# Kernel optimization log

Hardware: AMD Instinct MI355X
Metric: run time of the kernel (lower is better)

## Reference

```python
import jax, jax.numpy as jnp
import numpy as np

N_NODES = 100000


def gcn_conv(x, W, b, src, dst, n_nodes):
    # Linear transform first (PyG GCNConv applies weight before propagation)
    h = x @ W  # [N, out]
    # gcn_norm with self-loops: deg[i] = 1 + #incoming edges at i
    ones = jnp.ones(src.shape[0], dtype=h.dtype)
    deg = jax.ops.segment_sum(ones, dst, num_segments=n_nodes) + 1.0
    dinv = jax.lax.rsqrt(deg)  # deg^{-1/2}, deg >= 1 so safe
    norm = dinv[src] * dinv[dst]  # [E]
    # aggregate normalized messages at destination nodes
    agg = jax.ops.segment_sum(h[src] * norm[:, None], dst, num_segments=n_nodes)
    # self-loop contribution: norm_ii = dinv[i]^2
    agg = agg + h * (dinv * dinv)[:, None]
    return agg + b


def setup_inputs() -> dict:
    key = jax.random.key(0)
    k1, k2, k3, k4, k5, k6 = jax.random.split(key, 6)
    num_features, hidden, num_classes = 512, 128, 64
    x = jax.random.normal(k1, (N_NODES, num_features), dtype=jnp.float32)
    edge_index = jax.random.randint(k2, (2, 1600000), 0, N_NODES, dtype=jnp.int64)
    # Glorot-style params (scaled normals)
    W1 = jax.random.normal(k3, (num_features, hidden), dtype=jnp.float32) / np.sqrt(num_features)
    b1 = jnp.zeros((hidden,), dtype=jnp.float32)
    W2 = jax.random.normal(k4, (hidden, num_classes), dtype=jnp.float32) / np.sqrt(hidden)
    b2 = jnp.zeros((num_classes,), dtype=jnp.float32)
    return {"x": x, "edge_index": edge_index, "W1": W1, "b1": b1, "W2": W2, "b2": b2}


def reference(x, edge_index, W1, b1, W2, b2):
    src, dst = edge_index[0], edge_index[1]
    h = jax.nn.relu(gcn_conv(x, W1, b1, src, dst, N_NODES))
    out = gcn_conv(h, W2, b2, src, dst, N_NODES)
    return jax.nn.log_softmax(out, axis=1)
```

## Files before the change

### kernel.cpp

```cpp
#include <hip/hip_runtime.h>
#include <cmath>

#define N_NODES 100000
#define N_EDGES 1600000
#define F_IN 512
#define F_HID 128
#define F_OUT 64

#define SCAN_NB ((N_NODES + 255) / 256)

#define BK_SHIFT 10
#define NBUK ((N_NODES + 1023) >> 10)
#define SCAP 24576
#define LSLOT 64
#define NBLK_A 512
#define FILL_SPLIT 8
#define NPS (1024 / FILL_SPLIT)
#define OV_CAP 4096

typedef __attribute__((ext_vector_type(8))) short short8;
typedef __attribute__((ext_vector_type(4))) float float4v;

#define GLOAD_LDS16(g, l)                                                      \
    __builtin_amdgcn_global_load_lds(                                          \
        (const __attribute__((address_space(1))) void*)(g),                    \
        (__attribute__((address_space(3))) void*)(l), 16, 0, 0)

__device__ __forceinline__ unsigned short f2bf(float f) {
    unsigned u = __builtin_bit_cast(unsigned, f);
    u += 0x7FFFu + ((u >> 16) & 1u);
    return (unsigned short)(u >> 16);
}
__device__ __forceinline__ float bf2f(unsigned short s) {
    unsigned u = ((unsigned)s) << 16;
    return __builtin_bit_cast(float, u);
}
__device__ __forceinline__ float lo_bf(unsigned u) {
    return __builtin_bit_cast(float, u << 16);
}
__device__ __forceinline__ float hi_bf(unsigned u) {
    return __builtin_bit_cast(float, u & 0xFFFF0000u);
}
__device__ __forceinline__ short8 cvt8(float4 lo, float4 hi) {
    return short8{(short)f2bf(lo.x), (short)f2bf(lo.y), (short)f2bf(lo.z), (short)f2bf(lo.w),
                  (short)f2bf(hi.x), (short)f2bf(hi.y), (short)f2bf(hi.z), (short)f2bf(hi.w)};
}
__device__ __forceinline__ unsigned pack_bf2(float a, float b) {
    return (unsigned)f2bf(a) | ((unsigned)f2bf(b) << 16);
}

template <int N>
__device__ __forceinline__ void waitvm() {
    if constexpr (N == 0) asm volatile("s_waitcnt vmcnt(0)" ::: "memory");
    else if constexpr (N == 3) asm volatile("s_waitcnt vmcnt(3)" ::: "memory");
    else if constexpr (N == 6) asm volatile("s_waitcnt vmcnt(6)" ::: "memory");
    else static_assert(N == 0 || N == 3 || N == 6, "add literal");
}
#define LGKM0() asm volatile("s_waitcnt lgkmcnt(0)" ::: "memory")
#define BAR() __builtin_amdgcn_s_barrier()
#define SCHED0() __builtin_amdgcn_sched_barrier(0)

__global__ __launch_bounds__(256) void partition_kernel(
    const int* __restrict__ src, const int* __restrict__ dst,
    unsigned* __restrict__ staging, int* __restrict__ gcur,
    unsigned long long* __restrict__ ovbuf, int* __restrict__ ovcnt) {
    __shared__ unsigned buf[NBUK][LSLOT];
    __shared__ int cnt[NBUK];
    int tid = threadIdx.x;
    for (int b = tid; b < NBUK; b += 256) cnt[b] = 0;
    __syncthreads();
    constexpr int PER = (((N_EDGES + NBLK_A - 1) / NBLK_A) + 3) & ~3;
    int e0 = blockIdx.x * PER;
    int e1 = min(e0 + PER, N_EDGES);

    auto body = [&](int d, int s) {
        int b = d >> BK_SHIFT;
        unsigned rec = (unsigned)s | ((unsigned)(d & 1023) << 17);
        int slot = atomicAdd(&cnt[b], 1);
        if (slot < LSLOT) {
            buf[b][slot] = rec;
        } else {
            int op = atomicAdd(ovcnt, 1);
            if (op < OV_CAP)
                ovbuf[op] = ((unsigned long long)(unsigned)d << 32) | (unsigned)s;
        }
    };
    auto drain = [&](void) {
        for (int b = tid; b < NBUK; b += 256) {
            int c = min(cnt[b], LSLOT);
            int full = c & ~15;
            if (full > 0) {
                int pos = atomicAdd(&gcur[b], full);
                if (pos + full <= SCAP) {
                    unsigned* dp = &staging[(size_t)b * SCAP + pos];
                    for (int i = 0; i < full; ++i) dp[i] = buf[b][i];
                }
                for (int i = 0; i < c - full; ++i) buf[b][i] = buf[b][full + i];
            }
            cnt[b] = c - full;
        }
    };

    int base = e0;
    for (; base + 1024 <= e1; base += 1024) {
        int e = base + tid * 4;
        int4 dv = *(const int4*)(dst + e);
        int4 sv = *(const int4*)(src + e);
        body(dv.x, sv.x);
        body(dv.y, sv.y);
        body(dv.z, sv.z);
        body(dv.w, sv.w);
        __syncthreads();
        drain();
        __syncthreads();
    }
    for (int e = base + tid; e < e1; e += 256) body(dst[e], src[e]);
    __syncthreads();
    drain();
    __syncthreads();
    for (int b = tid; b < NBUK; b += 256) {
        int c = cnt[b];
        if (c > 0) {
            int pos = atomicAdd(&gcur[b], c);
            if (pos + c <= SCAP)
                for (int i = 0; i < c; ++i) staging[(size_t)b * SCAP + pos + i] = buf[b][i];
        }
    }
}

__global__ __launch_bounds__(256) void deg_hist_kernel(
    const unsigned* __restrict__ staging, const int* __restrict__ gcur,
    const unsigned long long* __restrict__ ovbuf, const int* __restrict__ ovcnt,
    int* __restrict__ deg) {
    int b = blockIdx.x;
    __shared__ int hist[1024];
    int tid = threadIdx.x;
    for (int i = tid; i < 1024; i += 256) hist[i] = 0;
    __syncthreads();
    int n = gcur[b];
    if (n > SCAP) n = SCAP;
    const unsigned* sp = &staging[(size_t)b * SCAP];
    int i = tid * 4;
    for (; i + 4 <= n; i += 1024) {
        uint4 r = *(const uint4*)(sp + i);
        atomicAdd(&hist[r.x >> 17], 1);
        atomicAdd(&hist[r.y >> 17], 1);
        atomicAdd(&hist[r.z >> 17], 1);
        atomicAdd(&hist[r.w >> 17], 1);
    }
    int tail0 = n & ~3;
    if (tid < (n - tail0)) atomicAdd(&hist[sp[tail0 + tid] >> 17], 1);
    int oc = *ovcnt;
    if (oc > OV_CAP) oc = OV_CAP;
    for (int k = tid; k < oc; k += 256) {
        int d = (int)(ovbuf[k] >> 32);
        if ((d >> BK_SHIFT) == b) atomicAdd(&hist[d & 1023], 1);
    }
    __syncthreads();
    int node0 = b << BK_SHIFT;
    for (int j = tid; j < 1024; j += 256) {
        int nd = node0 + j;
        if (nd < N_NODES) deg[nd] = hist[j];
    }
}

__global__ __launch_bounds__(256) void fill_kernel(
    const unsigned* __restrict__ staging, const int* __restrict__ gcur,
    const int* __restrict__ row_ptr, int* __restrict__ csr_src,
    const unsigned long long* __restrict__ ovbuf, const int* __restrict__ ovcnt) {
    int b = blockIdx.x / FILL_SPLIT;
    int slice = blockIdx.x - b * FILL_SPLIT;
    int dl0 = slice * NPS;
    int node0 = (b << BK_SHIFT) + dl0;
    __shared__ int lcur[NPS];
    int tid = threadIdx.x;
    if (tid < NPS) {
        int nd = node0 + tid;
        lcur[tid] = (nd < N_NODES) ? row_ptr[nd] : 0;
    }
    __syncthreads();

    int n = gcur[b];
    if (n > SCAP) n = SCAP;
    const unsigned* sp = &staging[(size_t)b * SCAP];

    auto process = [&](unsigned rec) {
        int dl = (int)(rec >> 17) - dl0;
        if ((unsigned)dl < (unsigned)NPS) {
            int pos = atomicAdd(&lcur[dl], 1);
            csr_src[pos] = (int)(rec & 0x1FFFFu);
        }
    };

    int i = tid * 4;
    for (; i + 4 <= n; i += 1024) {
        uint4 r = *(const uint4*)(sp + i);
        process(r.x);
        process(r.y);
        process(r.z);
        process(r.w);
    }
    int tail0 = n & ~3;
    if (tid < (n - tail0)) process(sp[tail0 + tid]);

    int oc = *ovcnt;
    if (oc > OV_CAP) oc = OV_CAP;
    for (int k = tid; k < oc; k += 256) {
        unsigned long long r = ovbuf[k];
        int d = (int)(r >> 32);
        int dl = d - node0;
        if ((d >> BK_SHIFT) == b && (unsigned)dl < (unsigned)NPS) {
            int pos = atomicAdd(&lcur[dl], 1);
            csr_src[pos] = (int)(r & 0xffffffffu);
        }
    }
}


__global__ __launch_bounds__(256) void block_sum_kernel(const int* __restrict__ deg,
                                                        int* __restrict__ bsum, int n) {
    int g = blockIdx.x * 256 + threadIdx.x;
    int v = (g < n) ? deg[g] : 0;
    __shared__ int ws[4];
    int lane = threadIdx.x & 63;
    int w = threadIdx.x >> 6;
#pragma unroll
    for (int o = 32; o > 0; o >>= 1) v += __shfl_down(v, o, 64);
    if (lane == 0) ws[w] = v;
    __syncthreads();
    if (threadIdx.x == 0) bsum[blockIdx.x] = ws[0] + ws[1] + ws[2] + ws[3];
}

__global__ __launch_bounds__(512) void scan_partials_kernel(int* __restrict__ bsum, int nb) {
    __shared__ int t[512];
    int tid = threadIdx.x;
    int v = (tid < nb) ? bsum[tid] : 0;
    t[tid] = v;
    __syncthreads();
    for (int d = 1; d < 512; d <<= 1) {
        int u = (tid >= d) ? t[tid - d] : 0;
        __syncthreads();
        t[tid] += u;
        __syncthreads();
    }
    if (tid < nb) bsum[tid] = t[tid] - v;
}

__global__ __launch_bounds__(256) void scan_final_kernel(const int* __restrict__ deg,
                                                         const int* __restrict__ bsum,
                                                         int* __restrict__ row_ptr,
                                                         float* __restrict__ dinv, int n) {
    __shared__ int t[256];
    int g = blockIdx.x * 256 + threadIdx.x;
    int tid = threadIdx.x;
    int v = (g < n) ? deg[g] : 0;
    t[tid] = v;
    __syncthreads();
    for (int d = 1; d < 256; d <<= 1) {
        int u = (tid >= d) ? t[tid - d] : 0;
        __syncthreads();
        t[tid] += u;
        __syncthreads();
    }
    int off = bsum[blockIdx.x] + t[tid] - v;
    if (g < n) {
        row_ptr[g] = off;
        dinv[g] = rsqrtf((float)(v + 1));
    }
    if (g == n - 1) row_ptr[n] = off + v;
}


__global__ void transpose_w_kernel(const float* __restrict__ W1, const float* __restrict__ W2,
                                   unsigned short* __restrict__ Wt1,
                                   unsigned short* __restrict__ Wt2) {
    int g = blockIdx.x * 256 + threadIdx.x;
    if (g < F_HID * F_IN) {
        int n = g >> 9, k = g & 511;
        Wt1[g] = f2bf(W1[k * F_HID + n]);
    } else {
        int h = g - F_HID * F_IN;
        if (h < F_OUT * F_HID) {
            int n = h >> 7, k = h & 127;
            Wt2[h] = f2bf(W2[k * F_OUT + n]);
        }
    }
}


template <int BN, int K, bool A_BF16>
__global__ __launch_bounds__(256, 3) void gemm_lds_kernel(
    const void* __restrict__ Araw, const unsigned short* __restrict__ Wt,
    const float* __restrict__ dinv, unsigned short* __restrict__ out, int N) {
    constexpr int NCT = BN / 16;
    constexpr int AE = A_BF16 ? 2 : 4;
    constexpr int SLOTS_A = (32 * AE) / 16;
    constexpr int MA = SLOTS_A - 1;
    constexpr int ABYTES = 128 * 32 * AE;
    constexpr int BBYTES = BN * 32 * 2;
    constexpr int NT = K / 32;
    constexpr int SL = (128 * SLOTS_A + BN * 4) / 256;

    __shared__ __align__(128) char Abuf[2][ABYTES];
    __shared__ __align__(128) char Bbuf[2][BBYTES];

    const char* Ab = (const char*)Araw;
    const char* Bb = (const char*)Wt;
    int tid = threadIdx.x;
    int lane = tid & 63;
    int wv = tid >> 6;
    int row0 = blockIdx.x * 128;
    int l15 = lane & 15;
    int q = lane >> 4;

    float4v acc[2][NCT] = {};

    auto stage = [&](int buf, int k0) {
        constexpr int CA = 128 * SLOTS_A;
#pragma unroll
        for (int i = 0; i < CA / 256; ++i) {
            int c = i * 256 + tid;
            int cw = i * 256 + (tid & ~63);
            int row = c / SLOTS_A;
            int s = c & MA;
            int g = s ^ (row & MA);
            int rg = row0 + row;
            if (rg >= N) rg = N - 1;
            GLOAD_LDS16(Ab + ((size_t)rg * K + k0) * AE + g * 16,
                        &Abuf[buf][cw * 16]);
        }
        constexpr int CB = BN * 4;
#pragma unroll
        for (int i = 0; i < CB / 256; ++i) {
            int c = i * 256 + tid;
            int cw = i * 256 + (tid & ~63);
            int col = c >> 2;
            int s = c & 3;
            int g = s ^ (col & 3);
            GLOAD_LDS16(Bb + ((size_t)col * K + k0) * 2 + g * 16,
                        &Bbuf[buf][cw * 16]);
        }
    };

    auto compute = [&](int buf) {
        const char* Ac = Abuf[buf];
        const char* Bc = Bbuf[buf];
        int lr0 = wv * 32 + l15;
        int lr1 = lr0 + 16;
        short8 a0, a1;
        if constexpr (A_BF16) {
            int s0 = q ^ (lr0 & 3);
            int s1 = q ^ (lr1 & 3);
            a0 = *(const short8*)(Ac + lr0 * 64 + s0 * 16);
            a1 = *(const short8*)(Ac + lr1 * 64 + s1 * 16);
        } else {
            int r7a = lr0 & 7, r7b = lr1 & 7;
            float4 f0 = *(const float4*)(Ac + lr0 * 128 + ((2 * q) ^ r7a) * 16);
            float4 f1 = *(const float4*)(Ac + lr0 * 128 + ((2 * q + 1) ^ r7a) * 16);
            float4 f2 = *(const float4*)(Ac + lr1 * 128 + ((2 * q) ^ r7b) * 16);
            float4 f3 = *(const float4*)(Ac + lr1 * 128 + ((2 * q + 1) ^ r7b) * 16);
            a0 = cvt8(f0, f1);
            a1 = cvt8(f2, f3);
        }
#pragma unroll
        for (int ct = 0; ct < NCT; ++ct) {
            int col = ct * 16 + l15;
            int sb = q ^ (col & 3);
            short8 b = *(const short8*)(Bc + col * 64 + sb * 16);
            acc[0][ct] = __builtin_amdgcn_mfma_f32_16x16x32_bf16(a0, b, acc[0][ct], 0, 0, 0);
            acc[1][ct] = __builtin_amdgcn_mfma_f32_16x16x32_bf16(a1, b, acc[1][ct], 0, 0, 0);
        }
    };

    stage(0, 0);
    stage(1, 32);
#pragma unroll 1
    for (int t = 0; t < NT - 2; ++t) {
        waitvm<SL>();
        BAR();
        SCHED0();
        compute(t & 1);
        LGKM0();
        BAR();
        SCHED0();
        stage(t & 1, (t + 2) * 32);
    }
    waitvm<SL>();
    BAR();
    SCHED0();
    compute((NT - 2) & 1);
    waitvm<0>();
    BAR();
    SCHED0();
    compute((NT - 1) & 1);

#pragma unroll
    for (int rt = 0; rt < 2; ++rt) {
#pragma unroll
        for (int reg = 0; reg < 4; ++reg) {
            int row = row0 + wv * 32 + rt * 16 + q * 4 + reg;
            if (row < N) {
                float sc = dinv[row];
#pragma unroll
                for (int ct = 0; ct < NCT; ++ct) {
                    out[(size_t)row * BN + ct * 16 + l15] = f2bf(acc[rt][ct][reg] * sc);
                }
            }
        }
    }
}


__global__ __launch_bounds__(256) void agg1_kernel(
    const uint4* __restrict__ g1v, const int* __restrict__ row_ptr,
    const int* __restrict__ csr_src, const float* __restrict__ dinv,
    const float4* __restrict__ b1v, uint4* __restrict__ h1v) {
    int tid = threadIdx.x;
    int wv = tid >> 6;
    int lane = tid & 63;
    int qt = lane >> 4;
    int ql = lane & 15;
    int node = blockIdx.x * 16 + wv * 4 + qt;
    uint4 u = g1v[(size_t)node * 16 + ql];
    float a0 = lo_bf(u.x), a1 = hi_bf(u.x), a2 = lo_bf(u.y), a3 = hi_bf(u.y);
    float a4 = lo_bf(u.z), a5 = hi_bf(u.z), a6 = lo_bf(u.w), a7 = hi_bf(u.w);
    int e = row_ptr[node], end = row_ptr[node + 1];
#define ACC8(v)                                                                \
    a0 += lo_bf(v.x); a1 += hi_bf(v.x); a2 += lo_bf(v.y); a3 += hi_bf(v.y);    \
    a4 += lo_bf(v.z); a5 += hi_bf(v.z); a6 += lo_bf(v.w); a7 += hi_bf(v.w)
    for (; e + 8 <= end; e += 8) {
        int j0 = csr_src[e + 0], j1 = csr_src[e + 1], j2 = csr_src[e + 2], j3 = csr_src[e + 3];
        int j4 = csr_src[e + 4], j5 = csr_src[e + 5], j6 = csr_src[e + 6], j7 = csr_src[e + 7];
        uint4 v0 = g1v[(size_t)j0 * 16 + ql];
        uint4 v1 = g1v[(size_t)j1 * 16 + ql];
        uint4 v2 = g1v[(size_t)j2 * 16 + ql];
        uint4 v3 = g1v[(size_t)j3 * 16 + ql];
        uint4 v4 = g1v[(size_t)j4 * 16 + ql];
        uint4 v5 = g1v[(size_t)j5 * 16 + ql];
        uint4 v6 = g1v[(size_t)j6 * 16 + ql];
        uint4 v7 = g1v[(size_t)j7 * 16 + ql];
        ACC8(v0); ACC8(v1); ACC8(v2); ACC8(v3);
        ACC8(v4); ACC8(v5); ACC8(v6); ACC8(v7);
    }
    for (; e + 2 <= end; e += 2) {
        uint4 v0 = g1v[(size_t)csr_src[e + 0] * 16 + ql];
        uint4 v1 = g1v[(size_t)csr_src[e + 1] * 16 + ql];
        ACC8(v0); ACC8(v1);
    }
    for (; e < end; ++e) {
        uint4 v0 = g1v[(size_t)csr_src[e] * 16 + ql];
        ACC8(v0);
    }
#undef ACC8
    float d = dinv[node];
    float4 ba = b1v[2 * ql], bb = b1v[2 * ql + 1];
    float r0 = fmaxf(d * a0 + ba.x, 0.0f), r1 = fmaxf(d * a1 + ba.y, 0.0f);
    float r2 = fmaxf(d * a2 + ba.z, 0.0f), r3 = fmaxf(d * a3 + ba.w, 0.0f);
    float r4 = fmaxf(d * a4 + bb.x, 0.0f), r5 = fmaxf(d * a5 + bb.y, 0.0f);
    float r6 = fmaxf(d * a6 + bb.z, 0.0f), r7 = fmaxf(d * a7 + bb.w, 0.0f);
    h1v[(size_t)node * 16 + ql] =
        uint4{pack_bf2(r0, r1), pack_bf2(r2, r3), pack_bf2(r4, r5), pack_bf2(r6, r7)};
}

__global__ __launch_bounds__(256) void agg2_lsm_kernel(
    const uint2* __restrict__ g2v, const int* __restrict__ row_ptr,
    const int* __restrict__ csr_src, const float* __restrict__ dinv,
    const float4* __restrict__ b2v, float4* __restrict__ outv) {
    int tid = threadIdx.x;
    int wv = tid >> 6;
    int lane = tid & 63;
    int qt = lane >> 4;
    int ql = lane & 15;
    int node = blockIdx.x * 16 + wv * 4 + qt;
    uint2 u = g2v[(size_t)node * 16 + ql];
    float a0 = lo_bf(u.x), a1 = hi_bf(u.x), a2 = lo_bf(u.y), a3 = hi_bf(u.y);
    int e = row_ptr[node], end = row_ptr[node + 1];
#define ACC4(v)                                                                \
    a0 += lo_bf(v.x); a1 += hi_bf(v.x); a2 += lo_bf(v.y); a3 += hi_bf(v.y)
    for (; e + 8 <= end; e += 8) {
        int j0 = csr_src[e + 0], j1 = csr_src[e + 1], j2 = csr_src[e + 2], j3 = csr_src[e + 3];
        int j4 = csr_src[e + 4], j5 = csr_src[e + 5], j6 = csr_src[e + 6], j7 = csr_src[e + 7];
        uint2 v0 = g2v[(size_t)j0 * 16 + ql];
        uint2 v1 = g2v[(size_t)j1 * 16 + ql];
        uint2 v2 = g2v[(size_t)j2 * 16 + ql];
        uint2 v3 = g2v[(size_t)j3 * 16 + ql];
        uint2 v4 = g2v[(size_t)j4 * 16 + ql];
        uint2 v5 = g2v[(size_t)j5 * 16 + ql];
        uint2 v6 = g2v[(size_t)j6 * 16 + ql];
        uint2 v7 = g2v[(size_t)j7 * 16 + ql];
        ACC4(v0); ACC4(v1); ACC4(v2); ACC4(v3);
        ACC4(v4); ACC4(v5); ACC4(v6); ACC4(v7);
    }
    for (; e + 2 <= end; e += 2) {
        uint2 v0 = g2v[(size_t)csr_src[e + 0] * 16 + ql];
        uint2 v1 = g2v[(size_t)csr_src[e + 1] * 16 + ql];
        ACC4(v0); ACC4(v1);
    }
    for (; e < end; ++e) {
        uint2 v0 = g2v[(size_t)csr_src[e] * 16 + ql];
        ACC4(v0);
    }
#undef ACC4
    float d = dinv[node];
    float4 b = b2v[ql];
    float v0 = d * a0 + b.x;
    float v1 = d * a1 + b.y;
    float v2 = d * a2 + b.z;
    float v3 = d * a3 + b.w;
    float m = fmaxf(fmaxf(v0, v1), fmaxf(v2, v3));
#pragma unroll
    for (int o = 8; o > 0; o >>= 1) m = fmaxf(m, __shfl_xor(m, o, 64));
    float s = __expf(v0 - m) + __expf(v1 - m) + __expf(v2 - m) + __expf(v3 - m);
#pragma unroll
    for (int o = 8; o > 0; o >>= 1) s += __shfl_xor(s, o, 64);
    float ls = m + __logf(s);
    outv[(size_t)node * 16 + ql] = float4{v0 - ls, v1 - ls, v2 - ls, v3 - ls};
}


extern "C" void kernel_launch(void* const* d_in, const int* in_sizes, int n_in,
                              void* d_out, int out_size, void* d_ws, size_t ws_size,
                              hipStream_t stream) {
    const float* x  = (const float*)d_in[0];
    const int* eidx = (const int*)d_in[1];
    const float* W1 = (const float*)d_in[2];
    const float* b1 = (const float*)d_in[3];
    const float* W2 = (const float*)d_in[4];
    const float* b2 = (const float*)d_in[5];
    float* out = (float*)d_out;
    const int* src = eidx;
    const int* dst = eidx + N_EDGES;

    char* base = (char*)d_ws;
    size_t off = 0;
    auto alloc = [&](size_t bytes) -> void* {
        void* p = base + off;
        off += (bytes + 255) & ~(size_t)255;
        return p;
    };
    int* zbase    = (int*)alloc((size_t)(NBUK + 64) * 4);
    int* gcur     = zbase;
    int* ovcnt    = zbase + NBUK;
    int* deg      = (int*)alloc((size_t)N_NODES * 4);
    int* row_ptr  = (int*)alloc((size_t)(N_NODES + 1) * 4);
    float* dinv   = (float*)alloc((size_t)N_NODES * 4);
    int* bsum     = (int*)alloc((size_t)SCAN_NB * 4);
    unsigned* staging = (unsigned*)alloc((size_t)NBUK * SCAP * 4);
    unsigned long long* ovbuf = (unsigned long long*)alloc((size_t)OV_CAP * 8);
    int* csr_src  = (int*)alloc((size_t)N_EDGES * 4);
    unsigned short* Wt1 = (unsigned short*)alloc((size_t)F_HID * F_IN * 2);
    unsigned short* Wt2 = (unsigned short*)alloc((size_t)F_OUT * F_HID * 2);
    unsigned short* g1  = (unsigned short*)alloc((size_t)N_NODES * F_HID * 2);
    unsigned short* h1  = (unsigned short*)alloc((size_t)N_NODES * F_HID * 2);
    unsigned short* g2  = g1;

    hipMemsetAsync(zbase, 0, (size_t)(NBUK + 64) * 4, stream);
    partition_kernel<<<NBLK_A, 256, 0, stream>>>(src, dst, staging, gcur, ovbuf, ovcnt);
    deg_hist_kernel<<<NBUK, 256, 0, stream>>>(staging, gcur, ovbuf, ovcnt, deg);
    block_sum_kernel<<<SCAN_NB, 256, 0, stream>>>(deg, bsum, N_NODES);
    scan_partials_kernel<<<1, 512, 0, stream>>>(bsum, SCAN_NB);
    scan_final_kernel<<<SCAN_NB, 256, 0, stream>>>(deg, bsum, row_ptr, dinv, N_NODES);
    fill_kernel<<<NBUK * FILL_SPLIT, 256, 0, stream>>>(staging, gcur, row_ptr, csr_src, ovbuf, ovcnt);
    transpose_w_kernel<<<(F_HID * F_IN + F_OUT * F_HID + 255) / 256, 256, 0, stream>>>(
        W1, W2, Wt1, Wt2);

    int gblocks = (N_NODES + 127) / 128;
    gemm_lds_kernel<F_HID, F_IN, false><<<gblocks, 256, 0, stream>>>(
        (const void*)x, Wt1, dinv, g1, N_NODES);
    agg1_kernel<<<N_NODES / 16, 256, 0, stream>>>(
        (const uint4*)g1, row_ptr, csr_src, dinv, (const float4*)b1, (uint4*)h1);

    gemm_lds_kernel<F_OUT, F_HID, true><<<gblocks, 256, 0, stream>>>(
        (const void*)h1, Wt2, dinv, g2, N_NODES);
    agg2_lsm_kernel<<<N_NODES / 16, 256, 0, stream>>>(
        (const uint2*)g2, row_ptr, csr_src, dinv, (const float4*)b2, (float4*)out);
}
```

Baseline: 500.9 us.

## Derive row offsets from bucket totals and software-pipeline gather loops

The global degree scan (block sum, partial scan, final scan) is replaced by a tiny single-block scan over per-bucket edge totals, so each bucket's histogram kernel computes its local prefix sum and writes row_ptr and dinv directly. This removes two kernel launches and the round trip of the deg array through memory. The aggregation kernels now prefetch the next eight gathered rows before accumulating the current ones, and they accumulate as packed float2 pairs so loads overlap with arithmetic. In exchange the gather loops hold more registers, and the scan depends on NBUK fitting in 128 threads.

```diff
diff --git a/kernel.cpp b/kernel.cpp
--- a/kernel.cpp
+++ b/kernel.cpp
@@ -6,8 +6,6 @@
 #define F_IN 512
 #define F_HID 128
 #define F_OUT 64
-
-#define SCAN_NB ((N_NODES + 255) / 256)
 
 #define BK_SHIFT 10
 #define NBUK ((N_NODES + 1023) >> 10)
@@ -20,6 +18,7 @@
 
 typedef __attribute__((ext_vector_type(8))) short short8;
 typedef __attribute__((ext_vector_type(4))) float float4v;
+typedef __attribute__((ext_vector_type(2))) float f2v;
 
 #define GLOAD_LDS16(g, l)                                                      \
     __builtin_amdgcn_global_load_lds(                                          \
@@ -31,15 +30,15 @@
     u += 0x7FFFu + ((u >> 16) & 1u);
     return (unsigned short)(u >> 16);
 }
-__device__ __forceinline__ float bf2f(unsigned short s) {
-    unsigned u = ((unsigned)s) << 16;
-    return __builtin_bit_cast(float, u);
-}
 __device__ __forceinline__ float lo_bf(unsigned u) {
     return __builtin_bit_cast(float, u << 16);
 }
 __device__ __forceinline__ float hi_bf(unsigned u) {
     return __builtin_bit_cast(float, u & 0xFFFF0000u);
+}
+__device__ __forceinline__ f2v bfpair(unsigned u) {
+    return f2v{__builtin_bit_cast(float, u << 16),
+               __builtin_bit_cast(float, u & 0xFFFF0000u)};
 }
 __device__ __forceinline__ short8 cvt8(float4 lo, float4 hi) {
     return short8{(short)f2bf(lo.x), (short)f2bf(lo.y), (short)f2bf(lo.z), (short)f2bf(lo.w),
@@ -128,12 +127,45 @@
     }
 }
 
-__global__ __launch_bounds__(256) void deg_hist_kernel(
+__global__ __launch_bounds__(128) void bucket_scan_kernel(
+    const int* __restrict__ gcur, const unsigned long long* __restrict__ ovbuf,
+    const int* __restrict__ ovcnt, int* __restrict__ bucket_base,
+    int* __restrict__ row_ptr) {
+    __shared__ int ovc[128];
+    __shared__ int sc[128];
+    int tid = threadIdx.x;
+    ovc[tid] = 0;
+    int tot = (tid < NBUK) ? min(gcur[tid], SCAP) : 0;
+    __syncthreads();
+    int oc = *ovcnt;
+    if (oc > OV_CAP) oc = OV_CAP;
+    for (int k = tid; k < oc; k += 128)
+        atomicAdd(&ovc[(int)(ovbuf[k] >> 32) >> BK_SHIFT], 1);
+    __syncthreads();
+    int v = tot + ovc[tid];
+    sc[tid] = v;
+    __syncthreads();
+    for (int d = 1; d < 128; d <<= 1) {
+        int u = (tid >= d) ? sc[tid - d] : 0;
+        __syncthreads();
+        sc[tid] += u;
+        __syncthreads();
+    }
+    if (tid < NBUK) bucket_base[tid] = sc[tid] - v;
+    if (tid == NBUK - 1) {
+        bucket_base[NBUK] = sc[tid];
+        row_ptr[N_NODES] = sc[tid];
+    }
+}
+
+__global__ __launch_bounds__(256) void deg_hist_row_kernel(
     const unsigned* __restrict__ staging, const int* __restrict__ gcur,
     const unsigned long long* __restrict__ ovbuf, const int* __restrict__ ovcnt,
-    int* __restrict__ deg) {
+    const int* __restrict__ bucket_base, int* __restrict__ row_ptr,
+    float* __restrict__ dinv) {
     int b = blockIdx.x;
     __shared__ int hist[1024];
+    __shared__ int psum[256];
     int tid = threadIdx.x;
     for (int i = tid; i < 1024; i += 256) hist[i] = 0;
     __syncthreads();
@@ -157,10 +189,28 @@
         if ((d >> BK_SHIFT) == b) atomicAdd(&hist[d & 1023], 1);
     }
     __syncthreads();
-    int node0 = b << BK_SHIFT;
-    for (int j = tid; j < 1024; j += 256) {
-        int nd = node0 + j;
-        if (nd < N_NODES) deg[nd] = hist[j];
+    int i4 = tid * 4;
+    int s0 = hist[i4], s1 = hist[i4 + 1], s2 = hist[i4 + 2], s3 = hist[i4 + 3];
+    int ms = s0 + s1 + s2 + s3;
+    psum[tid] = ms;
+    __syncthreads();
+    for (int d = 1; d < 256; d <<= 1) {
+        int u = (tid >= d) ? psum[tid - d] : 0;
+        __syncthreads();
+        psum[tid] += u;
+        __syncthreads();
+    }
+    int ex = psum[tid] - ms + bucket_base[b];
+    int nd = (b << BK_SHIFT) + i4;
+    if (nd < N_NODES) {
+        row_ptr[nd]     = ex;
+        row_ptr[nd + 1] = ex + s0;
+        row_ptr[nd + 2] = ex + s0 + s1;
+        row_ptr[nd + 3] = ex + s0 + s1 + s2;
+        dinv[nd]     = rsqrtf((float)(s0 + 1));
+        dinv[nd + 1] = rsqrtf((float)(s1 + 1));
+        dinv[nd + 2] = rsqrtf((float)(s2 + 1));
+        dinv[nd + 3] = rsqrtf((float)(s3 + 1));
     }
 }
 
@@ -214,60 +264,6 @@
             csr_src[pos] = (int)(r & 0xffffffffu);
         }
     }
-}
-
-
-__global__ __launch_bounds__(256) void block_sum_kernel(const int* __restrict__ deg,
-                                                        int* __restrict__ bsum, int n) {
-    int g = blockIdx.x * 256 + threadIdx.x;
-    int v = (g < n) ? deg[g] : 0;
-    __shared__ int ws[4];
-    int lane = threadIdx.x & 63;
-    int w = threadIdx.x >> 6;
-#pragma unroll
-    for (int o = 32; o > 0; o >>= 1) v += __shfl_down(v, o, 64);
-    if (lane == 0) ws[w] = v;
-    __syncthreads();
-    if (threadIdx.x == 0) bsum[blockIdx.x] = ws[0] + ws[1] + ws[2] + ws[3];
-}
-
-__global__ __launch_bounds__(512) void scan_partials_kernel(int* __restrict__ bsum, int nb) {
-    __shared__ int t[512];
-    int tid = threadIdx.x;
-    int v = (tid < nb) ? bsum[tid] : 0;
-    t[tid] = v;
-    __syncthreads();
-    for (int d = 1; d < 512; d <<= 1) {
-        int u = (tid >= d) ? t[tid - d] : 0;
-        __syncthreads();
-        t[tid] += u;
-        __syncthreads();
-    }
-    if (tid < nb) bsum[tid] = t[tid] - v;
-}
-
-__global__ __launch_bounds__(256) void scan_final_kernel(const int* __restrict__ deg,
-                                                         const int* __restrict__ bsum,
-                                                         int* __restrict__ row_ptr,
-                                                         float* __restrict__ dinv, int n) {
-    __shared__ int t[256];
-    int g = blockIdx.x * 256 + threadIdx.x;
-    int tid = threadIdx.x;
-    int v = (g < n) ? deg[g] : 0;
-    t[tid] = v;
-    __syncthreads();
-    for (int d = 1; d < 256; d <<= 1) {
-        int u = (tid >= d) ? t[tid - d] : 0;
-        __syncthreads();
-        t[tid] += u;
-        __syncthreads();
-    }
-    int off = bsum[blockIdx.x] + t[tid] - v;
-    if (g < n) {
-        row_ptr[g] = off;
-        dinv[g] = rsqrtf((float)(v + 1));
-    }
-    if (g == n - 1) row_ptr[n] = off + v;
 }
 
 
@@ -422,42 +418,41 @@
     int ql = lane & 15;
     int node = blockIdx.x * 16 + wv * 4 + qt;
     uint4 u = g1v[(size_t)node * 16 + ql];
-    float a0 = lo_bf(u.x), a1 = hi_bf(u.x), a2 = lo_bf(u.y), a3 = hi_bf(u.y);
-    float a4 = lo_bf(u.z), a5 = hi_bf(u.z), a6 = lo_bf(u.w), a7 = hi_bf(u.w);
+    f2v A0 = bfpair(u.x), A1 = bfpair(u.y), A2 = bfpair(u.z), A3 = bfpair(u.w);
     int e = row_ptr[node], end = row_ptr[node + 1];
-#define ACC8(v)                                                                \
-    a0 += lo_bf(v.x); a1 += hi_bf(v.x); a2 += lo_bf(v.y); a3 += hi_bf(v.y);    \
-    a4 += lo_bf(v.z); a5 += hi_bf(v.z); a6 += lo_bf(v.w); a7 += hi_bf(v.w)
-    for (; e + 8 <= end; e += 8) {
-        int j0 = csr_src[e + 0], j1 = csr_src[e + 1], j2 = csr_src[e + 2], j3 = csr_src[e + 3];
+#define GA1(j) g1v[(size_t)(j) * 16 + ql]
+#define ACCV(v)                                                                \
+    do { A0 += bfpair((v).x); A1 += bfpair((v).y);                             \
+         A2 += bfpair((v).z); A3 += bfpair((v).w); } while (0)
+    if (e + 8 <= end) {
+        int j0 = csr_src[e], j1 = csr_src[e + 1], j2 = csr_src[e + 2], j3 = csr_src[e + 3];
         int j4 = csr_src[e + 4], j5 = csr_src[e + 5], j6 = csr_src[e + 6], j7 = csr_src[e + 7];
-        uint4 v0 = g1v[(size_t)j0 * 16 + ql];
-        uint4 v1 = g1v[(size_t)j1 * 16 + ql];
-        uint4 v2 = g1v[(size_t)j2 * 16 + ql];
-        uint4 v3 = g1v[(size_t)j3 * 16 + ql];
-        uint4 v4 = g1v[(size_t)j4 * 16 + ql];
-        uint4 v5 = g1v[(size_t)j5 * 16 + ql];
-        uint4 v6 = g1v[(size_t)j6 * 16 + ql];
-        uint4 v7 = g1v[(size_t)j7 * 16 + ql];
-        ACC8(v0); ACC8(v1); ACC8(v2); ACC8(v3);
-        ACC8(v4); ACC8(v5); ACC8(v6); ACC8(v7);
-    }
-    for (; e + 2 <= end; e += 2) {
-        uint4 v0 = g1v[(size_t)csr_src[e + 0] * 16 + ql];
-        uint4 v1 = g1v[(size_t)csr_src[e + 1] * 16 + ql];
-        ACC8(v0); ACC8(v1);
+        uint4 v0 = GA1(j0), v1 = GA1(j1), v2 = GA1(j2), v3 = GA1(j3);
+        uint4 v4 = GA1(j4), v5 = GA1(j5), v6 = GA1(j6), v7 = GA1(j7);
+        e += 8;
+        for (; e + 8 <= end; e += 8) {
+            int k0 = csr_src[e], k1 = csr_src[e + 1], k2 = csr_src[e + 2], k3 = csr_src[e + 3];
+            int k4 = csr_src[e + 4], k5 = csr_src[e + 5], k6 = csr_src[e + 6], k7 = csr_src[e + 7];
+            ACCV(v0); ACCV(v1); ACCV(v2); ACCV(v3);
+            ACCV(v4); ACCV(v5); ACCV(v6); ACCV(v7);
+            v0 = GA1(k0); v1 = GA1(k1); v2 = GA1(k2); v3 = GA1(k3);
+            v4 = GA1(k4); v5 = GA1(k5); v6 = GA1(k6); v7 = GA1(k7);
+        }
+        ACCV(v0); ACCV(v1); ACCV(v2); ACCV(v3);
+        ACCV(v4); ACCV(v5); ACCV(v6); ACCV(v7);
     }
     for (; e < end; ++e) {
-        uint4 v0 = g1v[(size_t)csr_src[e] * 16 + ql];
-        ACC8(v0);
-    }
-#undef ACC8
+        uint4 v = GA1(csr_src[e]);
+        ACCV(v);
+    }
+#undef ACCV
+#undef GA1
     float d = dinv[node];
     float4 ba = b1v[2 * ql], bb = b1v[2 * ql + 1];
-    float r0 = fmaxf(d * a0 + ba.x, 0.0f), r1 = fmaxf(d * a1 + ba.y, 0.0f);
-    float r2 = fmaxf(d * a2 + ba.z, 0.0f), r3 = fmaxf(d * a3 + ba.w, 0.0f);
-    float r4 = fmaxf(d * a4 + bb.x, 0.0f), r5 = fmaxf(d * a5 + bb.y, 0.0f);
-    float r6 = fmaxf(d * a6 + bb.z, 0.0f), r7 = fmaxf(d * a7 + bb.w, 0.0f);
+    float r0 = fmaxf(d * A0.x + ba.x, 0.0f), r1 = fmaxf(d * A0.y + ba.y, 0.0f);
+    float r2 = fmaxf(d * A1.x + ba.z, 0.0f), r3 = fmaxf(d * A1.y + ba.w, 0.0f);
+    float r4 = fmaxf(d * A2.x + bb.x, 0.0f), r5 = fmaxf(d * A2.y + bb.y, 0.0f);
+    float r6 = fmaxf(d * A3.x + bb.z, 0.0f), r7 = fmaxf(d * A3.y + bb.w, 0.0f);
     h1v[(size_t)node * 16 + ql] =
         uint4{pack_bf2(r0, r1), pack_bf2(r2, r3), pack_bf2(r4, r5), pack_bf2(r6, r7)};
 }
@@ -473,40 +468,39 @@
     int ql = lane & 15;
     int node = blockIdx.x * 16 + wv * 4 + qt;
     uint2 u = g2v[(size_t)node * 16 + ql];
-    float a0 = lo_bf(u.x), a1 = hi_bf(u.x), a2 = lo_bf(u.y), a3 = hi_bf(u.y);
+    f2v A0 = bfpair(u.x), A1 = bfpair(u.y);
     int e = row_ptr[node], end = row_ptr[node + 1];
-#define ACC4(v)                                                                \
-    a0 += lo_bf(v.x); a1 += hi_bf(v.x); a2 += lo_bf(v.y); a3 += hi_bf(v.y)
-    for (; e + 8 <= end; e += 8) {
-        int j0 = csr_src[e + 0], j1 = csr_src[e + 1], j2 = csr_src[e + 2], j3 = csr_src[e + 3];
+#define GA2(j) g2v[(size_t)(j) * 16 + ql]
+#define ACCV(v) do { A0 += bfpair((v).x); A1 += bfpair((v).y); } while (0)
+    if (e + 8 <= end) {
+        int j0 = csr_src[e], j1 = csr_src[e + 1], j2 = csr_src[e + 2], j3 = csr_src[e + 3];
         int j4 = csr_src[e + 4], j5 = csr_src[e + 5], j6 = csr_src[e + 6], j7 = csr_src[e + 7];
-        uint2 v0 = g2v[(size_t)j0 * 16 + ql];
-        uint2 v1 = g2v[(size_t)j1 * 16 + ql];
-        uint2 v2 = g2v[(size_t)j2 * 16 + ql];
-        uint2 v3 = g2v[(size_t)j3 * 16 + ql];
-        uint2 v4 = g2v[(size_t)j4 * 16 + ql];
-        uint2 v5 = g2v[(size_t)j5 * 16 + ql];
-        uint2 v6 = g2v[(size_t)j6 * 16 + ql];
-        uint2 v7 = g2v[(size_t)j7 * 16 + ql];
-        ACC4(v0); ACC4(v1); ACC4(v2); ACC4(v3);
-        ACC4(v4); ACC4(v5); ACC4(v6); ACC4(v7);
-    }
-    for (; e + 2 <= end; e += 2) {
-        uint2 v0 = g2v[(size_t)csr_src[e + 0] * 16 + ql];
-        uint2 v1 = g2v[(size_t)csr_src[e + 1] * 16 + ql];
-        ACC4(v0); ACC4(v1);
+        uint2 v0 = GA2(j0), v1 = GA2(j1), v2 = GA2(j2), v3 = GA2(j3);
+        uint2 v4 = GA2(j4), v5 = GA2(j5), v6 = GA2(j6), v7 = GA2(j7);
+        e += 8;
+        for (; e + 8 <= end; e += 8) {
+            int k0 = csr_src[e], k1 = csr_src[e + 1], k2 = csr_src[e + 2], k3 = csr_src[e + 3];
+            int k4 = csr_src[e + 4], k5 = csr_src[e + 5], k6 = csr_src[e + 6], k7 = csr_src[e + 7];
+            ACCV(v0); ACCV(v1); ACCV(v2); ACCV(v3);
+            ACCV(v4); ACCV(v5); ACCV(v6); ACCV(v7);
+            v0 = GA2(k0); v1 = GA2(k1); v2 = GA2(k2); v3 = GA2(k3);
+            v4 = GA2(k4); v5 = GA2(k5); v6 = GA2(k6); v7 = GA2(k7);
+        }
+        ACCV(v0); ACCV(v1); ACCV(v2); ACCV(v3);
+        ACCV(v4); ACCV(v5); ACCV(v6); ACCV(v7);
     }
     for (; e < end; ++e) {
-        uint2 v0 = g2v[(size_t)csr_src[e] * 16 + ql];
-        ACC4(v0);
-    }
-#undef ACC4
+        uint2 v = GA2(csr_src[e]);
+        ACCV(v);
+    }
+#undef ACCV
+#undef GA2
     float d = dinv[node];
     float4 b = b2v[ql];
-    float v0 = d * a0 + b.x;
-    float v1 = d * a1 + b.y;
-    float v2 = d * a2 + b.z;
-    float v3 = d * a3 + b.w;
+    float v0 = d * A0.x + b.x;
+    float v1 = d * A0.y + b.y;
+    float v2 = d * A1.x + b.z;
+    float v3 = d * A1.y + b.w;
     float m = fmaxf(fmaxf(v0, v1), fmaxf(v2, v3));
 #pragma unroll
     for (int o = 8; o > 0; o >>= 1) m = fmaxf(m, __shfl_xor(m, o, 64));
@@ -541,10 +535,9 @@
     int* zbase    = (int*)alloc((size_t)(NBUK + 64) * 4);
     int* gcur     = zbase;
     int* ovcnt    = zbase + NBUK;
-    int* deg      = (int*)alloc((size_t)N_NODES * 4);
+    int* bucket_base = (int*)alloc((size_t)(NBUK + 1) * 4);
     int* row_ptr  = (int*)alloc((size_t)(N_NODES + 1) * 4);
     float* dinv   = (float*)alloc((size_t)N_NODES * 4);
-    int* bsum     = (int*)alloc((size_t)SCAN_NB * 4);
     unsigned* staging = (unsigned*)alloc((size_t)NBUK * SCAP * 4);
     unsigned long long* ovbuf = (unsigned long long*)alloc((size_t)OV_CAP * 8);
     int* csr_src  = (int*)alloc((size_t)N_EDGES * 4);
@@ -556,11 +549,11 @@
 
     hipMemsetAsync(zbase, 0, (size_t)(NBUK + 64) * 4, stream);
     partition_kernel<<<NBLK_A, 256, 0, stream>>>(src, dst, staging, gcur, ovbuf, ovcnt);
-    deg_hist_kernel<<<NBUK, 256, 0, stream>>>(staging, gcur, ovbuf, ovcnt, deg);
-    block_sum_kernel<<<SCAN_NB, 256, 0, stream>>>(deg, bsum, N_NODES);
-    scan_partials_kernel<<<1, 512, 0, stream>>>(bsum, SCAN_NB);
-    scan_final_kernel<<<SCAN_NB, 256, 0, stream>>>(deg, bsum, row_ptr, dinv, N_NODES);
-    fill_kernel<<<NBUK * FILL_SPLIT, 256, 0, stream>>>(staging, gcur, row_ptr, csr_src, ovbuf, ovcnt);
+    bucket_scan_kernel<<<1, 128, 0, stream>>>(gcur, ovbuf, ovcnt, bucket_base, row_ptr);
+    deg_hist_row_kernel<<<NBUK, 256, 0, stream>>>(staging, gcur, ovbuf, ovcnt,
+                                                  bucket_base, row_ptr, dinv);
+    fill_kernel<<<NBUK * FILL_SPLIT, 256, 0, stream>>>(staging, gcur, row_ptr, csr_src,
+                                                       ovbuf, ovcnt);
     transpose_w_kernel<<<(F_HID * F_IN + F_OUT * F_HID + 255) / 256, 256, 0, stream>>>(
         W1, W2, Wt1, Wt2);
 
```

Measured after the change: 504.0 us. No clear change (+0.6%).
